# Kernel tuning notes

Measured on AMD Instinct MI355X. Metric: run time of the kernel, lower is better.

The kernel has to match this reference:

```python
import jax, jax.numpy as jnp
import numpy as np

N_NODES = 100000
N_EDGES = 1600000
D = 64
BN_EPS = 1e-5


def setup_inputs() -> dict:
    key = jax.random.key(0)
    ks = jax.random.split(key, 10)
    s = 1.0 / np.sqrt(D)
    return {
        "features": jax.random.normal(ks[0], (N_NODES, D), dtype=jnp.float32),
        "src": jax.random.randint(ks[1], (N_EDGES,), 0, N_NODES, dtype=jnp.int32),
        "dst": jax.random.randint(ks[2], (N_EDGES,), 0, N_NODES, dtype=jnp.int32),
        "eps": jnp.zeros((), dtype=jnp.float32),
        "W1": jax.random.uniform(ks[3], (D, D), jnp.float32, -s, s),
        "b1": jax.random.uniform(ks[4], (D,), jnp.float32, -s, s),
        "W2": jax.random.uniform(ks[5], (D, D), jnp.float32, -s, s),
        "b2": jax.random.uniform(ks[6], (D,), jnp.float32, -s, s),
        "gamma": jnp.ones((D,), dtype=jnp.float32),
        "beta": jnp.zeros((D,), dtype=jnp.float32),
    }


def reference(features, src, dst, eps, W1, b1, W2, b2, gamma, beta):
    h_in = features
    # message passing: gather src node features, scatter-sum to dst (fn.copy_u + fn.sum)
    neigh = jax.ops.segment_sum(features[src], dst, num_segments=N_NODES)  # [N, D]
    # eps-weighted self term
    h = (1.0 + eps) * features + neigh
    # apply_func MLP: Linear -> ReLU -> Linear
    h = jnp.maximum(h @ W1 + b1, 0.0) @ W2 + b2
    # BatchNorm1d over nodes (training-mode batch statistics)
    mean = jnp.mean(h, axis=0)
    var = jnp.var(h, axis=0)
    h = (h - mean) * jax.lax.rsqrt(var + BN_EPS) * gamma + beta
    # activation
    h = jnp.maximum(h, 0.0)
    # residual (indim == outdim)
    h = h_in + h
    # dropout p=0 -> identity
    return h
```

## Files before the change

### kernel.cpp

```cpp
#include <hip/hip_runtime.h>
#include <hip/hip_fp16.h>

#define N_NODES 100000
#define N_EDGES 1600000
#define D 64
#define BN_EPS 1e-5f
#define NSHARD 32

#define NBKT 256
#define NPB 391
#define BKT_CAP 13056
#define NBBLK 391
#define SORT_T 1024

typedef _Float16 half8 __attribute__((ext_vector_type(8)));
typedef float f32x4 __attribute__((ext_vector_type(4)));

__global__ __launch_bounds__(256) void prep_k(
    const int* __restrict__ src, const int* __restrict__ dst,
    int* __restrict__ bkt_cnt, int* __restrict__ bktbuf,
    const float* __restrict__ feat, __half* __restrict__ feat16,
    const float* __restrict__ W1, const float* __restrict__ W2,
    _Float16* __restrict__ w1t, _Float16* __restrict__ w2t)
{
    __shared__ int h[NBKT], base[NBKT], cur[NBKT];
    const int blk = blockIdx.x;
    const int t = threadIdx.x;

    if (blk < NBBLK) {
        h[t] = 0; cur[t] = 0;
        __syncthreads();
        const int e0 = blk * 4096;
        int pk[16], b[16];
        #pragma unroll
        for (int i = 0; i < 16; ++i) {
            int e = e0 + i * 256 + t;
            if (e < N_EDGES) {
                int d = dst[e];
                b[i] = d / NPB;
                pk[i] = (src[e] << 9) | (d - b[i] * NPB);
                atomicAdd(&h[b[i]], 1);
            } else {
                b[i] = -1;
            }
        }
        __syncthreads();
        base[t] = atomicAdd(&bkt_cnt[t], h[t]);
        __syncthreads();
        #pragma unroll
        for (int i = 0; i < 16; ++i) {
            if (b[i] >= 0) {
                int p = atomicAdd(&cur[b[i]], 1);
                bktbuf[(size_t)b[i] * BKT_CAP + base[b[i]] + p] = pk[i];
            }
        }
    } else if (blk < NBBLK + 3125) {
        size_t i = ((size_t)(blk - NBBLK) * 256 + t) * 8;
        if (i < (size_t)N_NODES * D) {
            float4 v0 = *(const float4*)(feat + i);
            float4 v1 = *(const float4*)(feat + i + 4);
            __half2 o[4];
            o[0] = __floats2half2_rn(v0.x, v0.y);
            o[1] = __floats2half2_rn(v0.z, v0.w);
            o[2] = __floats2half2_rn(v1.x, v1.y);
            o[3] = __floats2half2_rn(v1.z, v1.w);
            *(float4*)(feat16 + i) = *(float4*)o;
        }
    } else {
        const int n = t >> 2;
        const int k0 = (t & 3) * 16;
        _Float16 o1[16], o2[16];
        #pragma unroll
        for (int j = 0; j < 16; ++j) {
            o1[j] = (_Float16)W1[(k0 + j) * 64 + n];
            o2[j] = (_Float16)W2[(k0 + j) * 64 + n];
        }
        #pragma unroll
        for (int j = 0; j < 16; j += 8) {
            *(half8*)(w1t + n * 64 + k0 + j) = *(half8*)&o1[j];
            *(half8*)(w2t + n * 64 + k0 + j) = *(half8*)&o2[j];
        }
    }
}

__device__ __forceinline__ int wscan_incl(int x, int lane)
{
    #pragma unroll
    for (int off = 1; off < 64; off <<= 1) {
        int v = __shfl_up(x, off, 64);
        if (lane >= off) x += v;
    }
    return x;
}

__global__ __launch_bounds__(SORT_T) void sortp_k(
    const int* __restrict__ bktbuf, const int* __restrict__ bkt_cnt,
    int* __restrict__ rowptr, int* __restrict__ col)
{
    __shared__ int h[NPB];
    __shared__ int cur[NPB];
    __shared__ int wsum[16];

    const int b    = blockIdx.x;
    const int t    = threadIdx.x;
    const int lane = t & 63;
    const int wv   = t >> 6;
    const int nb0  = b * NPB;
    const int nodes_in = min(NPB, N_NODES - nb0);
    const int cnt = min(bkt_cnt[b], BKT_CAP);
    const int* buf = bktbuf + (size_t)b * BKT_CAP;

    int ci = 0;
    if (t < NBKT && t < b) ci = min(bkt_cnt[t], BKT_CAP);
    #pragma unroll
    for (int off = 32; off >= 1; off >>= 1) ci += __shfl_xor(ci, off, 64);
    if (lane == 0) wsum[wv] = ci;
    if (t < NPB) h[t] = 0;
    __syncthreads();
    const int gbase = wsum[0] + wsum[1] + wsum[2] + wsum[3];

    for (int i = t; i < cnt; i += SORT_T)
        atomicAdd(&h[buf[i] & 511], 1);
    __syncthreads();

    int a = 0, x = 0;
    if (wv < 7) {
        a = (t < NPB) ? h[t] : 0;
        x = wscan_incl(a, lane);
        if (lane == 63) wsum[wv] = x;
    }
    __syncthreads();
    if (wv < 7) {
        int offs = 0;
        for (int i = 0; i < wv; ++i) offs += wsum[i];
        const int excl = x - a + offs;
        if (t < NPB) {
            cur[t] = excl;
            if (t < nodes_in) rowptr[nb0 + t] = gbase + excl;
        }
    }
    if (b == NBKT - 1 && t == 0) rowptr[N_NODES] = N_EDGES;
    __syncthreads();

    for (int i = t; i < cnt; i += SORT_T) {
        int pk = buf[i];
        int slot = atomicAdd(&cur[pk & 511], 1);
        col[gbase + slot] = pk >> 9;
    }
}

__device__ __forceinline__ void acc16(float* a, float4 r0, float4 r1)
{
    const __half2* h0 = (const __half2*)&r0;
    const __half2* h1 = (const __half2*)&r1;
    #pragma unroll
    for (int i = 0; i < 4; ++i) {
        float2 f = __half22float2(h0[i]);
        a[2 * i]     += f.x;
        a[2 * i + 1] += f.y;
    }
    #pragma unroll
    for (int i = 0; i < 4; ++i) {
        float2 f = __half22float2(h1[i]);
        a[8 + 2 * i]     += f.x;
        a[8 + 2 * i + 1] += f.y;
    }
}

__global__ __launch_bounds__(256) void gatherq_k(
    const __half* __restrict__ feat16, const int* __restrict__ rowptr,
    const int* __restrict__ col, const float* __restrict__ epsp,
    __half* __restrict__ x16)
{
    const int t = threadIdx.x;
    const int node = blockIdx.x * 64 + (t >> 2);
    if (node >= N_NODES) return;
    const int c = (t & 3) << 4;

    const int lo = rowptr[node];
    const int hi = rowptr[node + 1];

    float a[16];
    #pragma unroll
    for (int i = 0; i < 16; ++i) a[i] = 0.f;

    int e = lo;
    for (; e + 3 < hi; e += 4) {
        const int s0 = col[e], s1 = col[e + 1], s2 = col[e + 2], s3 = col[e + 3];
        const __half* p0 = feat16 + (size_t)s0 * 64 + c;
        const __half* p1 = feat16 + (size_t)s1 * 64 + c;
        const __half* p2 = feat16 + (size_t)s2 * 64 + c;
        const __half* p3 = feat16 + (size_t)s3 * 64 + c;
        float4 r00 = *(const float4*)(p0), r01 = *(const float4*)(p0 + 8);
        float4 r10 = *(const float4*)(p1), r11 = *(const float4*)(p1 + 8);
        float4 r20 = *(const float4*)(p2), r21 = *(const float4*)(p2 + 8);
        float4 r30 = *(const float4*)(p3), r31 = *(const float4*)(p3 + 8);
        acc16(a, r00, r01);
        acc16(a, r10, r11);
        acc16(a, r20, r21);
        acc16(a, r30, r31);
    }
    for (; e < hi; ++e) {
        const __half* p = feat16 + (size_t)col[e] * 64 + c;
        float4 r0 = *(const float4*)(p), r1 = *(const float4*)(p + 8);
        acc16(a, r0, r1);
    }

    const float epsv = 1.0f + epsp[0];
    const size_t gb = (size_t)node * 64 + c;
    float4 s0 = *(const float4*)(feat16 + gb);
    float4 s1 = *(const float4*)(feat16 + gb + 8);
    const __half2* h0 = (const __half2*)&s0;
    const __half2* h1 = (const __half2*)&s1;
    __half2 o[8];
    #pragma unroll
    for (int i = 0; i < 4; ++i) {
        float2 f = __half22float2(h0[i]);
        o[i] = __floats2half2_rn(fmaf(epsv, f.x, a[2 * i]),
                                 fmaf(epsv, f.y, a[2 * i + 1]));
    }
    #pragma unroll
    for (int i = 0; i < 4; ++i) {
        float2 f = __half22float2(h1[i]);
        o[4 + i] = __floats2half2_rn(fmaf(epsv, f.x, a[8 + 2 * i]),
                                     fmaf(epsv, f.y, a[8 + 2 * i + 1]));
    }
    *(float4*)(x16 + gb)     = *(float4*)&o[0];
    *(float4*)(x16 + gb + 8) = *(float4*)&o[4];
}

__global__ __launch_bounds__(256) void mfma_mlp2_k(
    const __half* __restrict__ x16,
    const _Float16* __restrict__ w1t, const _Float16* __restrict__ w2t,
    const float* __restrict__ b1, const float* __restrict__ b2,
    __half* __restrict__ h216, float* __restrict__ stats)
{
    __shared__ __align__(16) _Float16 xts[64 * 72];
    __shared__ float bnred[4 * 128];

    const int t    = threadIdx.x;
    const int w    = t >> 6;
    const int lane = t & 63;
    const int m    = lane & 15;
    const int q    = lane >> 4;
    const int rbase = w * 16;
    const int nb   = blockIdx.x * 64;

    const _Float16* xg = (const _Float16*)x16 + (size_t)(nb + rbase + m) * 64 + q * 8;
    half8 a0 = *(const half8*)(xg);
    half8 a1 = *(const half8*)(xg + 32);

    f32x4 acc[4];
    #pragma unroll
    for (int jt = 0; jt < 4; ++jt) {
        const float bias = b1[jt * 16 + m];
        acc[jt] = (f32x4){bias, bias, bias, bias};
        const _Float16* bw = w1t + (jt * 16 + m) * 64 + q * 8;
        half8 bf0 = *(const half8*)(bw);
        half8 bf1 = *(const half8*)(bw + 32);
        acc[jt] = __builtin_amdgcn_mfma_f32_16x16x32_f16(a0, bf0, acc[jt], 0, 0, 0);
        acc[jt] = __builtin_amdgcn_mfma_f32_16x16x32_f16(a1, bf1, acc[jt], 0, 0, 0);
    }

    #pragma unroll
    for (int jt = 0; jt < 4; ++jt)
        #pragma unroll
        for (int r = 0; r < 4; ++r)
            xts[(rbase + q * 4 + r) * 72 + jt * 16 + m] =
                (_Float16)fmaxf(acc[jt][r], 0.0f);
    asm volatile("s_waitcnt lgkmcnt(0)" ::: "memory");
    __builtin_amdgcn_sched_barrier(0);

    const _Float16* xw = &xts[(rbase + m) * 72 + q * 8];
    half8 c0 = *(const half8*)(xw);
    half8 c1 = *(const half8*)(xw + 32);

    f32x4 acc2[4];
    #pragma unroll
    for (int jt = 0; jt < 4; ++jt) {
        const float bias = b2[jt * 16 + m];
        acc2[jt] = (f32x4){bias, bias, bias, bias};
        const _Float16* bw = w2t + (jt * 16 + m) * 64 + q * 8;
        half8 bf0 = *(const half8*)(bw);
        half8 bf1 = *(const half8*)(bw + 32);
        acc2[jt] = __builtin_amdgcn_mfma_f32_16x16x32_f16(c0, bf0, acc2[jt], 0, 0, 0);
        acc2[jt] = __builtin_amdgcn_mfma_f32_16x16x32_f16(c1, bf1, acc2[jt], 0, 0, 0);
    }
    asm volatile("s_waitcnt lgkmcnt(0)" ::: "memory");
    __builtin_amdgcn_sched_barrier(0);

    float psums[4], psqs[4];
    #pragma unroll
    for (int jt = 0; jt < 4; ++jt) {
        float ps = 0.f, pq = 0.f;
        #pragma unroll
        for (int r = 0; r < 4; ++r) {
            const int row = rbase + q * 4 + r;
            const float v = acc2[jt][r];
            const float vv = (nb + row < N_NODES) ? v : 0.f;
            ps += vv;
            pq += vv * vv;
            xts[row * 72 + jt * 16 + m] = (_Float16)v;
        }
        ps += __shfl_xor(ps, 16, 64); ps += __shfl_xor(ps, 32, 64);
        pq += __shfl_xor(pq, 16, 64); pq += __shfl_xor(pq, 32, 64);
        psums[jt] = ps; psqs[jt] = pq;
    }
    if (lane < 16) {
        #pragma unroll
        for (int jt = 0; jt < 4; ++jt) {
            bnred[w * 128 + jt * 16 + lane]      = psums[jt];
            bnred[w * 128 + 64 + jt * 16 + lane] = psqs[jt];
        }
    }
    asm volatile("s_waitcnt lgkmcnt(0)" ::: "memory");
    __builtin_amdgcn_sched_barrier(0);

    {
        const int rr = lane >> 2;
        const int cc = (lane & 3) * 16;
        const int gn = nb + rbase + rr;
        if (gn < N_NODES) {
            float4 r0 = *(const float4*)&xts[(rbase + rr) * 72 + cc];
            float4 r1 = *(const float4*)&xts[(rbase + rr) * 72 + cc + 8];
            *(float4*)(h216 + (size_t)gn * 64 + cc)     = r0;
            *(float4*)(h216 + (size_t)gn * 64 + cc + 8) = r1;
        }
    }

    __syncthreads();
    if (t < 128) {
        const float v = bnred[t] + bnred[128 + t] + bnred[256 + t] + bnred[384 + t];
        unsafeAtomicAdd(stats + (size_t)(blockIdx.x & (NSHARD - 1)) * 128 + t, v);
    }
}

__global__ __launch_bounds__(256) void finish16_k(
    const float* __restrict__ feat, const __half* __restrict__ h216,
    const float* __restrict__ stats, const float* __restrict__ gamma,
    const float* __restrict__ beta, float* __restrict__ out)
{
    __shared__ float raw[128];
    __shared__ float scs[64], shs[64];
    const int t = threadIdx.x;
    if (t < 128) {
        float s = 0.f;
        #pragma unroll
        for (int c = 0; c < NSHARD; ++c)
            s += stats[c * 128 + t];
        raw[t] = s;
    }
    __syncthreads();
    if (t < 64) {
        const float invN = 1.0f / (float)N_NODES;
        const float mean = raw[t] * invN;
        const float var  = raw[64 + t] * invN - mean * mean;
        const float scale = gamma[t] * rsqrtf(var + BN_EPS);
        scs[t] = scale;
        shs[t] = beta[t] - mean * scale;
    }
    __syncthreads();
    size_t i = (size_t)blockIdx.x * 256 + t;
    if (i < (size_t)N_NODES * D / 4) {
        int j = (int)((i * 4) & 63);
        const __half2* hp = (const __half2*)(h216 + i * 4);
        float2 h0 = __half22float2(hp[0]);
        float2 h1 = __half22float2(hp[1]);
        float4 f = *(const float4*)(feat + i * 4);
        float4 o;
        o.x = fmaxf(fmaf(h0.x, scs[j + 0], shs[j + 0]), 0.f) + f.x;
        o.y = fmaxf(fmaf(h0.y, scs[j + 1], shs[j + 1]), 0.f) + f.y;
        o.z = fmaxf(fmaf(h1.x, scs[j + 2], shs[j + 2]), 0.f) + f.z;
        o.w = fmaxf(fmaf(h1.y, scs[j + 3], shs[j + 3]), 0.f) + f.w;
        *(float4*)(out + i * 4) = o;
    }
}

#define OCAP 7680

__global__ void bnstats_k(const float* __restrict__ stats,
                          const float* __restrict__ gamma,
                          const float* __restrict__ beta,
                          float* __restrict__ sf)
{
    int j = threadIdx.x;
    float s = 0.f, q = 0.f;
    for (int c = 0; c < NSHARD; ++c) {
        s += stats[c * 128 + j];
        q += stats[c * 128 + 64 + j];
    }
    const float invN = 1.0f / (float)N_NODES;
    float mean  = s * invN;
    float var   = q * invN - mean * mean;
    float scale = gamma[j] * rsqrtf(var + BN_EPS);
    sf[j]      = scale;
    sf[64 + j] = beta[j] - mean * scale;
}

__global__ __launch_bounds__(256) void bucket2_k(
    const int* __restrict__ src, const int* __restrict__ dst,
    int* __restrict__ bkt_cnt, int2* __restrict__ bktbuf)
{
    __shared__ int h[NBKT], base[NBKT], cur[NBKT];
    const int t = threadIdx.x;
    h[t] = 0; cur[t] = 0;
    __syncthreads();
    const int e0 = blockIdx.x * 4096;
    int s[16], d[16], b[16];
    #pragma unroll
    for (int i = 0; i < 16; ++i) {
        int e = e0 + i * 256 + t;
        if (e < N_EDGES) {
            s[i] = src[e];
            d[i] = dst[e];
            b[i] = d[i] / NPB;
            atomicAdd(&h[b[i]], 1);
        } else {
            b[i] = -1;
        }
    }
    __syncthreads();
    base[t] = atomicAdd(&bkt_cnt[t], h[t]);
    __syncthreads();
    #pragma unroll
    for (int i = 0; i < 16; ++i) {
        if (b[i] >= 0) {
            int p = atomicAdd(&cur[b[i]], 1);
            bktbuf[(size_t)b[i] * OCAP + base[b[i]] + p] = make_int2(s[i], d[i]);
        }
    }
}

__global__ __launch_bounds__(SORT_T) void sort2_k(
    const int2* __restrict__ bktbuf, const int* __restrict__ bkt_cnt,
    int* __restrict__ rowptr, int* __restrict__ col)
{
    __shared__ int h[NPB];
    __shared__ int cur[NPB];
    __shared__ int part[SORT_T];
    __shared__ int bsc[NBKT];

    const int b = blockIdx.x;
    const int t = threadIdx.x;
    const int nb0 = b * NPB;
    const int nodes_in = min(NPB, N_NODES - nb0);
    const int cnt = bkt_cnt[b];
    const int2* buf = bktbuf + (size_t)b * OCAP;

    if (t < NBKT) bsc[t] = bkt_cnt[t];
    __syncthreads();
    for (int off = 1; off < NBKT; off <<= 1) {
        int x = 0;
        if (t < NBKT) {
            x = bsc[t];
            if (t >= off) x += bsc[t - off];
        }
        __syncthreads();
        if (t < NBKT) bsc[t] = x;
        __syncthreads();
    }
    const int gbase = bsc[b] - cnt;

    if (t < NPB) h[t] = 0;
    __syncthreads();

    for (int i = t; i < cnt; i += SORT_T)
        atomicAdd(&h[buf[i].y - nb0], 1);
    __syncthreads();

    int a = (t < NPB) ? h[t] : 0;
    part[t] = a;
    __syncthreads();
    for (int off = 1; off < SORT_T; off <<= 1) {
        int x = part[t];
        int u = (t >= off) ? part[t - off] : 0;
        __syncthreads();
        part[t] = x + u;
        __syncthreads();
    }
    int excl = part[t] - a;
    if (t < NPB) {
        cur[t] = excl;
        if (t < nodes_in) rowptr[nb0 + t] = gbase + excl;
    }
    if (b == NBKT - 1 && t == 0) rowptr[N_NODES] = N_EDGES;
    __syncthreads();

    for (int i = t; i < cnt; i += SORT_T) {
        int2 r = buf[i];
        int slot = atomicAdd(&cur[r.y - nb0], 1);
        col[gbase + slot] = r.x;
    }
}

__global__ __launch_bounds__(256) void gather32_k(
    const float* __restrict__ feat, const int* __restrict__ rowptr,
    const int* __restrict__ col, const float* __restrict__ epsp,
    float* __restrict__ x)
{
    int node = blockIdx.x * 4 + (threadIdx.x >> 6);
    int lane = threadIdx.x & 63;
    if (node >= N_NODES) return;
    int g = lane >> 4;
    int c = (lane & 15) << 2;
    int lo = rowptr[node];
    int hi = rowptr[node + 1];
    float ax = 0.f, ay = 0.f, az = 0.f, aw = 0.f;
    int e = lo + g;
    for (; e + 4 < hi; e += 8) {
        int s0 = col[e];
        int s1 = col[e + 4];
        float4 v0 = *(const float4*)(feat + (size_t)s0 * D + c);
        float4 v1 = *(const float4*)(feat + (size_t)s1 * D + c);
        ax += v0.x; ay += v0.y; az += v0.z; aw += v0.w;
        ax += v1.x; ay += v1.y; az += v1.z; aw += v1.w;
    }
    if (e < hi) {
        float4 v = *(const float4*)(feat + (size_t)col[e] * D + c);
        ax += v.x; ay += v.y; az += v.z; aw += v.w;
    }
    #pragma unroll
    for (int off = 16; off <= 32; off <<= 1) {
        ax += __shfl_xor(ax, off, 64);
        ay += __shfl_xor(ay, off, 64);
        az += __shfl_xor(az, off, 64);
        aw += __shfl_xor(aw, off, 64);
    }
    if (g == 0) {
        float4 f = *(const float4*)(feat + (size_t)node * D + c);
        const float epsv = 1.0f + epsp[0];
        float4 r;
        r.x = fmaf(epsv, f.x, ax);
        r.y = fmaf(epsv, f.y, ay);
        r.z = fmaf(epsv, f.z, az);
        r.w = fmaf(epsv, f.w, aw);
        *(float4*)(x + (size_t)node * D + c) = r;
    }
}

__global__ __launch_bounds__(256) void mlp32_k(
    const float* __restrict__ x,
    const float* __restrict__ W1, const float* __restrict__ b1,
    const float* __restrict__ W2, const float* __restrict__ b2,
    float* __restrict__ h2out, float* __restrict__ stats)
{
    __shared__ float W1s[64 * 68];
    __shared__ float W2s[64 * 68];
    __shared__ float xs[64 * 65];
    __shared__ float b1s[64], b2s[64];

    const int t  = threadIdx.x;
    const int nb = blockIdx.x * 64;

    #pragma unroll
    for (int i = 0; i < 4; ++i) {
        int l  = t + i * 256;
        int k  = l >> 4;
        int j4 = (l & 15) << 2;
        *(float4*)(&W1s[k * 68 + j4]) = *(const float4*)(W1 + k * 64 + j4);
        *(float4*)(&W2s[k * 68 + j4]) = *(const float4*)(W2 + k * 64 + j4);
    }
    if (t < 64)       b1s[t]      = b1[t];
    else if (t < 128) b2s[t - 64] = b2[t - 64];

    #pragma unroll
    for (int i = 0; i < 2; ++i) {
        int n  = (t >> 3) + i * 32;
        int k8 = (t & 7) << 3;
        int gn = nb + n;
        float4 a = make_float4(0.f, 0.f, 0.f, 0.f), b = a;
        if (gn < N_NODES) {
            a = *(const float4*)(x + (size_t)gn * D + k8);
            b = *(const float4*)(x + (size_t)gn * D + k8 + 4);
        }
        *(float4*)&xs[n * 65 + k8]     = a;
        *(float4*)&xs[n * 65 + k8 + 4] = b;
    }
    __syncthreads();

    const int n0 = (t & 15) << 2;
    const int j0 = (t >> 4) << 2;
    const float* xr0 = &xs[(n0 + 0) * 65];
    const float* xr1 = &xs[(n0 + 1) * 65];
    const float* xr2 = &xs[(n0 + 2) * 65];
    const float* xr3 = &xs[(n0 + 3) * 65];

    float acc[4][4];
    #pragma unroll
    for (int a = 0; a < 4; ++a)
        #pragma unroll
        for (int b = 0; b < 4; ++b)
            acc[a][b] = b1s[j0 + b];

    #pragma unroll 8
    for (int k = 0; k < 64; ++k) {
        const float4 w = *(const float4*)(&W1s[k * 68 + j0]);
        const float x0 = xr0[k], x1 = xr1[k], x2 = xr2[k], x3 = xr3[k];
        acc[0][0] = fmaf(x0, w.x, acc[0][0]); acc[0][1] = fmaf(x0, w.y, acc[0][1]);
        acc[0][2] = fmaf(x0, w.z, acc[0][2]); acc[0][3] = fmaf(x0, w.w, acc[0][3]);
        acc[1][0] = fmaf(x1, w.x, acc[1][0]); acc[1][1] = fmaf(x1, w.y, acc[1][1]);
        acc[1][2] = fmaf(x1, w.z, acc[1][2]); acc[1][3] = fmaf(x1, w.w, acc[1][3]);
        acc[2][0] = fmaf(x2, w.x, acc[2][0]); acc[2][1] = fmaf(x2, w.y, acc[2][1]);
        acc[2][2] = fmaf(x2, w.z, acc[2][2]); acc[2][3] = fmaf(x2, w.w, acc[2][3]);
        acc[3][0] = fmaf(x3, w.x, acc[3][0]); acc[3][1] = fmaf(x3, w.y, acc[3][1]);
        acc[3][2] = fmaf(x3, w.z, acc[3][2]); acc[3][3] = fmaf(x3, w.w, acc[3][3]);
    }

    __syncthreads();
    #pragma unroll
    for (int a = 0; a < 4; ++a)
        #pragma unroll
        for (int b = 0; b < 4; ++b)
            xs[(n0 + a) * 65 + j0 + b] = fmaxf(acc[a][b], 0.0f);
    __syncthreads();

    float acc2[4][4];
    #pragma unroll
    for (int a = 0; a < 4; ++a)
        #pragma unroll
        for (int b = 0; b < 4; ++b)
            acc2[a][b] = b2s[j0 + b];

    #pragma unroll 8
    for (int k = 0; k < 64; ++k) {
        const float4 w = *(const float4*)(&W2s[k * 68 + j0]);
        const float x0 = xr0[k], x1 = xr1[k], x2 = xr2[k], x3 = xr3[k];
        acc2[0][0] = fmaf(x0, w.x, acc2[0][0]); acc2[0][1] = fmaf(x0, w.y, acc2[0][1]);
        acc2[0][2] = fmaf(x0, w.z, acc2[0][2]); acc2[0][3] = fmaf(x0, w.w, acc2[0][3]);
        acc2[1][0] = fmaf(x1, w.x, acc2[1][0]); acc2[1][1] = fmaf(x1, w.y, acc2[1][1]);
        acc2[1][2] = fmaf(x1, w.z, acc2[1][2]); acc2[1][3] = fmaf(x1, w.w, acc2[1][3]);
        acc2[2][0] = fmaf(x2, w.x, acc2[2][0]); acc2[2][1] = fmaf(x2, w.y, acc2[2][1]);
        acc2[2][2] = fmaf(x2, w.z, acc2[2][2]); acc2[2][3] = fmaf(x2, w.w, acc2[2][3]);
        acc2[3][0] = fmaf(x3, w.x, acc2[3][0]); acc2[3][1] = fmaf(x3, w.y, acc2[3][1]);
        acc2[3][2] = fmaf(x3, w.z, acc2[3][2]); acc2[3][3] = fmaf(x3, w.w, acc2[3][3]);
    }

    float psum[4] = {0.f, 0.f, 0.f, 0.f};
    float psq[4]  = {0.f, 0.f, 0.f, 0.f};
    #pragma unroll
    for (int a = 0; a < 4; ++a) {
        int gn = nb + n0 + a;
        if (gn < N_NODES) {
            float4 hh;
            hh.x = acc2[a][0]; hh.y = acc2[a][1]; hh.z = acc2[a][2]; hh.w = acc2[a][3];
            *(float4*)(h2out + (size_t)gn * 64 + j0) = hh;
            psum[0] += hh.x; psq[0] += hh.x * hh.x;
            psum[1] += hh.y; psq[1] += hh.y * hh.y;
            psum[2] += hh.z; psq[2] += hh.z * hh.z;
            psum[3] += hh.w; psq[3] += hh.w * hh.w;
        }
    }
    #pragma unroll
    for (int off = 8; off >= 1; off >>= 1)
        #pragma unroll
        for (int b = 0; b < 4; ++b) {
            psum[b] += __shfl_down(psum[b], off, 16);
            psq[b]  += __shfl_down(psq[b],  off, 16);
        }
    if ((t & 15) == 0) {
        float* sp = stats + (size_t)(blockIdx.x & (NSHARD - 1)) * 128;
        #pragma unroll
        for (int b = 0; b < 4; ++b) {
            unsafeAtomicAdd(sp + j0 + b,      psum[b]);
            unsafeAtomicAdd(sp + 64 + j0 + b, psq[b]);
        }
    }
}

__global__ __launch_bounds__(256) void finish_k(
    const float* __restrict__ feat, const float* __restrict__ sf,
    float* __restrict__ out)
{
    __shared__ float scs[64], shs[64];
    if (threadIdx.x < 64) {
        scs[threadIdx.x] = sf[threadIdx.x];
        shs[threadIdx.x] = sf[64 + threadIdx.x];
    }
    __syncthreads();
    size_t i = (size_t)blockIdx.x * 256 + threadIdx.x;
    if (i < (size_t)N_NODES * D / 4) {
        int j = (int)((i * 4) & 63);
        float4 h = *(float4*)(out + i * 4);
        float4 f = *(const float4*)(feat + i * 4);
        h.x = fmaxf(fmaf(h.x, scs[j + 0], shs[j + 0]), 0.f) + f.x;
        h.y = fmaxf(fmaf(h.y, scs[j + 1], shs[j + 1]), 0.f) + f.y;
        h.z = fmaxf(fmaf(h.z, scs[j + 2], shs[j + 2]), 0.f) + f.z;
        h.w = fmaxf(fmaf(h.w, scs[j + 3], shs[j + 3]), 0.f) + f.w;
        *(float4*)(out + i * 4) = h;
    }
}

extern "C" void kernel_launch(void* const* d_in, const int* in_sizes, int n_in,
                              void* d_out, int out_size, void* d_ws, size_t ws_size,
                              hipStream_t stream)
{
    const float* feat  = (const float*)d_in[0];
    const int*   src   = (const int*)d_in[1];
    const int*   dst   = (const int*)d_in[2];
    const float* eps   = (const float*)d_in[3];
    const float* W1    = (const float*)d_in[4];
    const float* b1    = (const float*)d_in[5];
    const float* W2    = (const float*)d_in[6];
    const float* b2    = (const float*)d_in[7];
    const float* gamma = (const float*)d_in[8];
    const float* beta  = (const float*)d_in[9];
    float* out = (float*)d_out;

    const size_t BKTSZ  = (size_t)NBKT * BKT_CAP * sizeof(int);
    const size_t F16SZ  = (size_t)N_NODES * D * sizeof(__half);
    const size_t COLSZ  = (size_t)N_EDGES * sizeof(int);
    const size_t RPSZ   = ((size_t)(N_NODES + 1) * sizeof(int) + 15) & ~(size_t)15;
    const size_t STATSZ = (size_t)NSHARD * 128 * sizeof(float);
    const size_t CNTSZ  = (size_t)NBKT * sizeof(int);
    const size_t TAIL   = STATSZ + CNTSZ + 128 * 4 + 2 * 4096 * sizeof(_Float16) + 256;
    const size_t need   = BKTSZ + F16SZ + COLSZ + RPSZ + TAIL;

    if (ws_size >= need) {
        char* p = (char*)d_ws;
        int*    bktbuf  = (int*)p;
        __half* x16     = (__half*)p;
        __half* feat16  = (__half*)(p + BKTSZ);
        __half* h216    = feat16;
        int*    col     = (int*)(p + BKTSZ + F16SZ);
        int*    rowptr  = (int*)(p + BKTSZ + F16SZ + COLSZ);
        float*  stats   = (float*)(p + BKTSZ + F16SZ + COLSZ + RPSZ);
        int*    bkt_cnt = (int*)(stats + NSHARD * 128);
        float*  sf      = (float*)(bkt_cnt + NBKT);
        _Float16* w1t   = (_Float16*)(sf + 128);
        _Float16* w2t   = w1t + 4096;
        (void)sf;

        hipMemsetAsync(stats, 0, STATSZ + CNTSZ, stream);
        prep_k<<<NBBLK + 3125 + 1, 256, 0, stream>>>(src, dst, bkt_cnt, bktbuf,
                                                     feat, feat16, W1, W2, w1t, w2t);
        sortp_k<<<NBKT, SORT_T, 0, stream>>>(bktbuf, bkt_cnt, rowptr, col);
        gatherq_k<<<(N_NODES + 63) / 64, 256, 0, stream>>>(feat16, rowptr, col, eps, x16);
        mfma_mlp2_k<<<(N_NODES + 63) / 64, 256, 0, stream>>>(x16, w1t, w2t, b1, b2, h216, stats);
        finish16_k<<<(N_NODES * D / 4 + 255) / 256, 256, 0, stream>>>(
            feat, h216, stats, gamma, beta, out);
    } else {
        const size_t X32SZ = (size_t)N_NODES * D * sizeof(float);
        char* p = (char*)d_ws;
        float* x32    = (float*)p;
        int2*  bktbuf = (int2*)p;
        int*   col    = (int*)(p + X32SZ);
        int*   rowptr = col + N_EDGES;
        float* stats  = (float*)(rowptr + N_NODES + 1);
        int*   bkt_cnt = (int*)(stats + NSHARD * 128);
        float* sf     = (float*)(bkt_cnt + NBKT);

        hipMemsetAsync(stats, 0, STATSZ + NBKT * 4, stream);
        bucket2_k<<<(N_EDGES + 4095) / 4096, 256, 0, stream>>>(src, dst, bkt_cnt, bktbuf);
        sort2_k<<<NBKT, SORT_T, 0, stream>>>(bktbuf, bkt_cnt, rowptr, col);
        gather32_k<<<(N_NODES + 3) / 4, 256, 0, stream>>>(feat, rowptr, col, eps, x32);
        mlp32_k<<<(N_NODES + 63) / 64, 256, 0, stream>>>(x32, W1, b1, W2, b2, out, stats);
        bnstats_k<<<1, 64, 0, stream>>>(stats, gamma, beta, sf);
        finish_k<<<(N_NODES * D / 4 + 255) / 256, 256, 0, stream>>>(feat, sf, out);
    }
}
```

Baseline: 197.5 us.

## Fuse MLP and BatchNorm finish via grid-wide barrier; stage sorted columns in LDS

Merges the MLP kernel and the BatchNorm/residual finish kernel into one kernel. Blocks publish partial statistics, then spin on a global atomic counter until every block has arrived, and then apply normalization directly from LDS. This removes the fp16 h2 round trip through global memory and one kernel launch. The sort kernel now builds col in a shared-memory staging buffer for coalesced writes, and it zeroes the stats array itself, so the memset shrinks to bkt_cnt plus the counter. The grid barrier needs all 1563 blocks to be co-resident, otherwise it deadlocks. The launch-bounds hint of 7 is meant to help with that, but it raises register pressure.

```diff
diff --git a/kernel.cpp b/kernel.cpp
--- a/kernel.cpp
+++ b/kernel.cpp
@@ -95,11 +95,12 @@
 
 __global__ __launch_bounds__(SORT_T) void sortp_k(
     const int* __restrict__ bktbuf, const int* __restrict__ bkt_cnt,
-    int* __restrict__ rowptr, int* __restrict__ col)
+    int* __restrict__ rowptr, int* __restrict__ col, float* __restrict__ stats)
 {
     __shared__ int h[NPB];
     __shared__ int cur[NPB];
     __shared__ int wsum[16];
+    __shared__ int colstage[BKT_CAP];
 
     const int b    = blockIdx.x;
     const int t    = threadIdx.x;
@@ -110,6 +111,10 @@
     const int cnt = min(bkt_cnt[b], BKT_CAP);
     const int* buf = bktbuf + (size_t)b * BKT_CAP;
 
+    if (b == 0) {
+        for (int i = t; i < NSHARD * 128; i += SORT_T) stats[i] = 0.f;
+    }
+
     int ci = 0;
     if (t < NBKT && t < b) ci = min(bkt_cnt[t], BKT_CAP);
     #pragma unroll
@@ -145,8 +150,11 @@
     for (int i = t; i < cnt; i += SORT_T) {
         int pk = buf[i];
         int slot = atomicAdd(&cur[pk & 511], 1);
-        col[gbase + slot] = pk >> 9;
-    }
+        colstage[slot] = pk >> 9;
+    }
+    __syncthreads();
+    for (int i = t; i < cnt; i += SORT_T)
+        col[gbase + i] = colstage[i];
 }
 
 __device__ __forceinline__ void acc16(float* a, float4 r0, float4 r1)
@@ -229,14 +237,17 @@
     *(float4*)(x16 + gb + 8) = *(float4*)&o[4];
 }
 
-__global__ __launch_bounds__(256) void mfma_mlp2_k(
+__global__ __launch_bounds__(256, 7) void mlpfin_k(
     const __half* __restrict__ x16,
     const _Float16* __restrict__ w1t, const _Float16* __restrict__ w2t,
     const float* __restrict__ b1, const float* __restrict__ b2,
-    __half* __restrict__ h216, float* __restrict__ stats)
+    const float* __restrict__ feat, const float* __restrict__ gamma,
+    const float* __restrict__ beta, float* __restrict__ out,
+    float* __restrict__ stats, int* __restrict__ counter)
 {
     __shared__ __align__(16) _Float16 xts[64 * 72];
     __shared__ float bnred[4 * 128];
+    __shared__ float scs[64], shs[64];
 
     const int t    = threadIdx.x;
     const int w    = t >> 6;
@@ -313,9 +324,40 @@
             bnred[w * 128 + 64 + jt * 16 + lane] = psqs[jt];
         }
     }
-    asm volatile("s_waitcnt lgkmcnt(0)" ::: "memory");
-    __builtin_amdgcn_sched_barrier(0);
-
+
+    __syncthreads();
+    if (t < 128) {
+        const float v = bnred[t] + bnred[128 + t] + bnred[256 + t] + bnred[384 + t];
+        unsafeAtomicAdd(stats + (size_t)(blockIdx.x & (NSHARD - 1)) * 128 + t, v);
+    }
+    __threadfence();
+    __syncthreads();
+
+    if (t == 0) {
+        __hip_atomic_fetch_add(counter, 1, __ATOMIC_ACQ_REL, __HIP_MEMORY_SCOPE_AGENT);
+        while (__hip_atomic_load(counter, __ATOMIC_ACQUIRE, __HIP_MEMORY_SCOPE_AGENT)
+               < (int)gridDim.x) {}
+    }
+    __syncthreads();
+
+    if (t < 128) {
+        float s = 0.f;
+        #pragma unroll
+        for (int c = 0; c < NSHARD; ++c)
+            s += __hip_atomic_load(stats + c * 128 + t, __ATOMIC_RELAXED,
+                                   __HIP_MEMORY_SCOPE_AGENT);
+        bnred[t] = s;
+    }
+    __syncthreads();
+    if (t < 64) {
+        const float invN = 1.0f / (float)N_NODES;
+        const float mean = bnred[t] * invN;
+        const float var  = bnred[64 + t] * invN - mean * mean;
+        const float scale = gamma[t] * rsqrtf(var + BN_EPS);
+        scs[t] = scale;
+        shs[t] = beta[t] - mean * scale;
+    }
+    __syncthreads();
     {
         const int rr = lane >> 2;
         const int cc = (lane & 3) * 16;
@@ -323,56 +365,35 @@
         if (gn < N_NODES) {
             float4 r0 = *(const float4*)&xts[(rbase + rr) * 72 + cc];
             float4 r1 = *(const float4*)&xts[(rbase + rr) * 72 + cc + 8];
-            *(float4*)(h216 + (size_t)gn * 64 + cc)     = r0;
-            *(float4*)(h216 + (size_t)gn * 64 + cc + 8) = r1;
-        }
-    }
-
-    __syncthreads();
-    if (t < 128) {
-        const float v = bnred[t] + bnred[128 + t] + bnred[256 + t] + bnred[384 + t];
-        unsafeAtomicAdd(stats + (size_t)(blockIdx.x & (NSHARD - 1)) * 128 + t, v);
-    }
-}
-
-__global__ __launch_bounds__(256) void finish16_k(
-    const float* __restrict__ feat, const __half* __restrict__ h216,
-    const float* __restrict__ stats, const float* __restrict__ gamma,
-    const float* __restrict__ beta, float* __restrict__ out)
-{
-    __shared__ float raw[128];
-    __shared__ float scs[64], shs[64];
-    const int t = threadIdx.x;
-    if (t < 128) {
-        float s = 0.f;
-        #pragma unroll
-        for (int c = 0; c < NSHARD; ++c)
-            s += stats[c * 128 + t];
-        raw[t] = s;
-    }
-    __syncthreads();
-    if (t < 64) {
-        const float invN = 1.0f / (float)N_NODES;
-        const float mean = raw[t] * invN;
-        const float var  = raw[64 + t] * invN - mean * mean;
-        const float scale = gamma[t] * rsqrtf(var + BN_EPS);
-        scs[t] = scale;
-        shs[t] = beta[t] - mean * scale;
-    }
-    __syncthreads();
-    size_t i = (size_t)blockIdx.x * 256 + t;
-    if (i < (size_t)N_NODES * D / 4) {
-        int j = (int)((i * 4) & 63);
-        const __half2* hp = (const __half2*)(h216 + i * 4);
-        float2 h0 = __half22float2(hp[0]);
-        float2 h1 = __half22float2(hp[1]);
-        float4 f = *(const float4*)(feat + i * 4);
-        float4 o;
-        o.x = fmaxf(fmaf(h0.x, scs[j + 0], shs[j + 0]), 0.f) + f.x;
-        o.y = fmaxf(fmaf(h0.y, scs[j + 1], shs[j + 1]), 0.f) + f.y;
-        o.z = fmaxf(fmaf(h1.x, scs[j + 2], shs[j + 2]), 0.f) + f.z;
-        o.w = fmaxf(fmaf(h1.y, scs[j + 3], shs[j + 3]), 0.f) + f.w;
-        *(float4*)(out + i * 4) = o;
+            const __half2* hh0 = (const __half2*)&r0;
+            const __half2* hh1 = (const __half2*)&r1;
+            const float* frow = feat + (size_t)gn * 64 + cc;
+            float* orow = out + (size_t)gn * 64 + cc;
+            #pragma unroll
+            for (int i = 0; i < 2; ++i) {
+                float4 f0 = *(const float4*)(frow + i * 8);
+                float4 f1 = *(const float4*)(frow + i * 8 + 4);
+                float2 ha = __half22float2(hh0[i * 2 + (i == 0 ? 0 : 0)]);
+                const __half2* hp = (i == 0) ? hh0 : hh1;
+                float2 v0 = __half22float2(hp[0]);
+                float2 v1 = __half22float2(hp[1]);
+                float2 v2 = __half22float2(hp[2]);
+                float2 v3 = __half22float2(hp[3]);
+                const int j = cc + i * 8;
+                float4 o0, o1;
+                o0.x = fmaxf(fmaf(v0.x, scs[j + 0], shs[j + 0]), 0.f) + f0.x;
+                o0.y = fmaxf(fmaf(v0.y, scs[j + 1], shs[j + 1]), 0.f) + f0.y;
+                o0.z = fmaxf(fmaf(v1.x, scs[j + 2], shs[j + 2]), 0.f) + f0.z;
+                o0.w = fmaxf(fmaf(v1.y, scs[j + 3], shs[j + 3]), 0.f) + f0.w;
+                o1.x = fmaxf(fmaf(v2.x, scs[j + 4], shs[j + 4]), 0.f) + f1.x;
+                o1.y = fmaxf(fmaf(v2.y, scs[j + 5], shs[j + 5]), 0.f) + f1.y;
+                o1.z = fmaxf(fmaf(v3.x, scs[j + 6], shs[j + 6]), 0.f) + f1.z;
+                o1.w = fmaxf(fmaf(v3.y, scs[j + 7], shs[j + 7]), 0.f) + f1.w;
+                *(float4*)(orow + i * 8)     = o0;
+                *(float4*)(orow + i * 8 + 4) = o1;
+                (void)ha;
+            }
+        }
     }
 }
 
@@ -712,7 +733,7 @@
     const size_t RPSZ   = ((size_t)(N_NODES + 1) * sizeof(int) + 15) & ~(size_t)15;
     const size_t STATSZ = (size_t)NSHARD * 128 * sizeof(float);
     const size_t CNTSZ  = (size_t)NBKT * sizeof(int);
-    const size_t TAIL   = STATSZ + CNTSZ + 128 * 4 + 2 * 4096 * sizeof(_Float16) + 256;
+    const size_t TAIL   = STATSZ + CNTSZ + 128 * 4 + 2 * 4096 * sizeof(_Float16) + 512;
     const size_t need   = BKTSZ + F16SZ + COLSZ + RPSZ + TAIL;
 
     if (ws_size >= need) {
@@ -720,24 +741,21 @@
         int*    bktbuf  = (int*)p;
         __half* x16     = (__half*)p;
         __half* feat16  = (__half*)(p + BKTSZ);
-        __half* h216    = feat16;
         int*    col     = (int*)(p + BKTSZ + F16SZ);
         int*    rowptr  = (int*)(p + BKTSZ + F16SZ + COLSZ);
         float*  stats   = (float*)(p + BKTSZ + F16SZ + COLSZ + RPSZ);
         int*    bkt_cnt = (int*)(stats + NSHARD * 128);
-        float*  sf      = (float*)(bkt_cnt + NBKT);
-        _Float16* w1t   = (_Float16*)(sf + 128);
+        int*    counter = bkt_cnt + NBKT;
+        _Float16* w1t   = (_Float16*)(counter + 16);
         _Float16* w2t   = w1t + 4096;
-        (void)sf;
-
-        hipMemsetAsync(stats, 0, STATSZ + CNTSZ, stream);
+
+        hipMemsetAsync(bkt_cnt, 0, CNTSZ + 64, stream);
         prep_k<<<NBBLK + 3125 + 1, 256, 0, stream>>>(src, dst, bkt_cnt, bktbuf,
                                                      feat, feat16, W1, W2, w1t, w2t);
-        sortp_k<<<NBKT, SORT_T, 0, stream>>>(bktbuf, bkt_cnt, rowptr, col);
+        sortp_k<<<NBKT, SORT_T, 0, stream>>>(bktbuf, bkt_cnt, rowptr, col, stats);
         gatherq_k<<<(N_NODES + 63) / 64, 256, 0, stream>>>(feat16, rowptr, col, eps, x16);
-        mfma_mlp2_k<<<(N_NODES + 63) / 64, 256, 0, stream>>>(x16, w1t, w2t, b1, b2, h216, stats);
-        finish16_k<<<(N_NODES * D / 4 + 255) / 256, 256, 0, stream>>>(
-            feat, h216, stats, gamma, beta, out);
+        mlpfin_k<<<(N_NODES + 63) / 64, 256, 0, stream>>>(
+            x16, w1t, w2t, b1, b2, feat, gamma, beta, out, stats, counter);
     } else {
         const size_t X32SZ = (size_t)N_NODES * D * sizeof(float);
         char* p = (char*)d_ws;
```

After: 493.0 us. 150% more time.
